# Kernel tuning notes

Measured on AMD Instinct MI355X. Metric: run time of the kernel, lower is better.

## Reference

```python
import jax, jax.numpy as jnp
import numpy as np

B, S, D, N = 8, 4096, 1024, 16
EPS = 1e-6


def setup_inputs() -> dict:
    key = jax.random.key(0)
    ks = jax.random.split(key, 6)
    s = 1.0 / np.sqrt(D)
    return {
        "x": jax.random.normal(ks[0], (B, S, D), dtype=jnp.float32),
        "W_lambda": jax.random.uniform(ks[1], (N, D), jnp.float32, -s, s),
        "b_lambda": jnp.full((N,), 2.0, dtype=jnp.float32),  # nn.init.constant_(bias, 2.0)
        "W_B": jax.random.uniform(ks[2], (N, D), jnp.float32, -s, s),
        "W_C": jax.random.uniform(ks[3], (D, N), jnp.float32, -1.0 / np.sqrt(N), 1.0 / np.sqrt(N)),
        "W_gate": jax.random.uniform(ks[4], (D, D), jnp.float32, -s, s),
        "rms_weight": jnp.ones((D,), dtype=jnp.float32),
    }


def reference(x, W_lambda, b_lambda, W_B, W_C, W_gate, rms_weight):
    # Input-dependent decay and input projection, computed for all timesteps at once
    lam = jax.nn.sigmoid(jnp.einsum("bsd,nd->bsn", x, W_lambda) + b_lambda)  # (B,S,N)
    Bx = jnp.einsum("bsd,nd->bsn", x, W_B)  # (B,S,N)

    def step(h, inp):
        l_t, b_t = inp
        h = l_t * h + b_t  # h_t = lambda_t * h_{t-1} + B_t x_t
        return h, h

    h0 = jnp.zeros((x.shape[0], W_B.shape[0]), dtype=x.dtype)
    _, hs = jax.lax.scan(step, h0, (jnp.swapaxes(lam, 0, 1), jnp.swapaxes(Bx, 0, 1)))
    hs = jnp.swapaxes(hs, 0, 1)  # (B,S,N)

    y = jnp.einsum("bsn,dn->bsd", hs, W_C)  # C @ h_t
    gate = jax.nn.sigmoid(jnp.einsum("bsd,ed->bse", x, W_gate))
    y = gate * y
    # RMSNorm
    rms = jax.lax.rsqrt(jnp.mean(y * y, axis=-1, keepdims=True) + EPS)
    return y * rms * rms_weight
```

## Files before the change

### kernel.cpp

```cpp
#include <hip/hip_runtime.h>

#define DD 1024
#define NN 16
#define SS 4096
#define BBATCH 8
#define TOK (BBATCH*SS)

typedef __attribute__((ext_vector_type(8))) __bf16 bf16x8;
typedef __attribute__((ext_vector_type(4))) float f32x4;
typedef unsigned int u32;
typedef unsigned long long u64;

__device__ __forceinline__ void async16(void* lds, const void* g) {
  __builtin_amdgcn_global_load_lds(
      (const __attribute__((address_space(1))) u32*)(u64)(g),
      (__attribute__((address_space(3))) u32*)(u32)(u64)(lds), 16, 0, 0);
}

__device__ __forceinline__ float sigmoidf_(float v) {
  return 1.f / (1.f + __expf(-v));
}

__global__ void k_cvt(const float* __restrict__ in, __bf16* __restrict__ out, int n8) {
  int i = blockIdx.x * blockDim.x + threadIdx.x;
  if (i >= n8) return;
  const float4* in4 = (const float4*)in;
  float4 a = in4[(u64)i * 2 + 0];
  float4 b = in4[(u64)i * 2 + 1];
  bf16x8 o;
  o[0] = (__bf16)a.x; o[1] = (__bf16)a.y; o[2] = (__bf16)a.z; o[3] = (__bf16)a.w;
  o[4] = (__bf16)b.x; o[5] = (__bf16)b.y; o[6] = (__bf16)b.z; o[7] = (__bf16)b.w;
  *(bf16x8*)(out + (u64)i * 8) = o;
}

__global__ __launch_bounds__(256)
void k_proj(const __bf16* __restrict__ xb, const __bf16* __restrict__ wp,
            const float* __restrict__ b_lambda,
            float* __restrict__ lam, float* __restrict__ bx) {
  __shared__ __align__(16) __bf16 sA[128 * 32];
  __shared__ __align__(16) __bf16 sB[32 * 32];
  int tid = threadIdx.x;
  int lane = tid & 63, w = tid >> 6;
  int tok0 = blockIdx.x * 128;
  u64 aSrc[2];
#pragma unroll
  for (int q = 0; q < 2; ++q) {
    int u = q * 256 + tid;
    int row = u >> 2, slot = (u & 3) ^ (row & 3);
    aSrc[q] = (u64)((const char*)xb + ((u64)(tok0 + row) * DD + slot * 8) * 2);
  }
  u64 bSrc;
  {
    int u = tid;
    int row = u >> 2, slot = (u & 3) ^ (row & 3);
    bSrc = (u64)((const char*)wp + ((u64)row * DD + slot * 8) * 2);
  }
  f32x4 acc[2][2] = {};
  int r15 = lane & 15, kg = lane >> 4;
  for (int kt = 0; kt < DD / 32; ++kt) {
#pragma unroll
    for (int q = 0; q < 2; ++q)
      async16((char*)sA + (q * 256 + w * 64) * 16, (const void*)(aSrc[q] + kt * 64));
    if (tid < 128)
      async16((char*)sB + w * 1024, (const void*)(bSrc + kt * 64));
    __syncthreads();
    bf16x8 bfr[2];
#pragma unroll
    for (int nt = 0; nt < 2; ++nt) {
      int brow = nt * 16 + r15;
      bfr[nt] = *(const bf16x8*)((const char*)sB + brow * 64 + ((kg ^ (brow & 3)) << 4));
    }
#pragma unroll
    for (int mt = 0; mt < 2; ++mt) {
      int arow = w * 32 + mt * 16 + r15;
      bf16x8 af = *(const bf16x8*)((const char*)sA + arow * 64 + ((kg ^ (arow & 3)) << 4));
#pragma unroll
      for (int nt = 0; nt < 2; ++nt)
        acc[mt][nt] = __builtin_amdgcn_mfma_f32_16x16x32_bf16(af, bfr[nt], acc[mt][nt], 0, 0, 0);
    }
    __syncthreads();
  }
#pragma unroll
  for (int mt = 0; mt < 2; ++mt)
#pragma unroll
    for (int nt = 0; nt < 2; ++nt)
#pragma unroll
      for (int r = 0; r < 4; ++r) {
        int token = tok0 + w * 32 + mt * 16 + kg * 4 + r;
        int j = nt * 16 + r15;
        float v = acc[mt][nt][r];
        if (j < 16) lam[token * NN + j] = sigmoidf_(v + b_lambda[j]);
        else        bx[token * NN + (j - 16)] = v;
      }
}

__global__ __launch_bounds__(256)
void k_scan(const float* __restrict__ lam, const float* __restrict__ bx,
            float* __restrict__ hs) {
  int b = blockIdx.x >> 4, n = blockIdx.x & 15;
  int t = threadIdx.x;
  const int CH = SS / 256;
  float lv[CH], bv[CH];
  int base = (b * SS + t * CH) * NN + n;
  float a = 1.f, bacc = 0.f;
#pragma unroll
  for (int i = 0; i < CH; ++i) {
    lv[i] = lam[base + i * NN];
    bv[i] = bx[base + i * NN];
    bacc = lv[i] * bacc + bv[i];
    a *= lv[i];
  }
  __shared__ float As[2][256], Bs[2][256];
  As[0][t] = a; Bs[0][t] = bacc;
  __syncthreads();
  int cur = 0;
  for (int off = 1; off < 256; off <<= 1) {
    float a2 = As[cur][t], b2 = Bs[cur][t];
    if (t >= off) {
      float ap = As[cur][t - off], bp = Bs[cur][t - off];
      b2 = b2 + a2 * bp;
      a2 = a2 * ap;
    }
    As[cur ^ 1][t] = a2; Bs[cur ^ 1][t] = b2;
    cur ^= 1;
    __syncthreads();
  }
  float h = (t == 0) ? 0.f : Bs[cur][t - 1];
#pragma unroll
  for (int i = 0; i < CH; ++i) {
    h = lv[i] * h + bv[i];
    hs[base + i * NN] = h;
  }
}

#define STG(kt, bi) do { u32 lb = (u32)(bi) * 32768u; u64 ko = (u64)(kt) * 64u;          \
    async16(smc + lb + (u32)w * 1024u,              (const void*)(aAddr0 + ko));         \
    async16(smc + lb + (u32)(8 + w) * 1024u,        (const void*)(aAddr1 + ko));         \
    async16(smc + lb + 16384u + (u32)w * 1024u,     (const void*)(bAddr0 + ko));         \
    async16(smc + lb + 16384u + (u32)(8 + w) * 1024u,(const void*)(bAddr1 + ko)); } while (0)

__global__ __launch_bounds__(512, 2)
void k_gemm(const __bf16* __restrict__ xb, const __bf16* __restrict__ wg,
            const float* __restrict__ hs, const float* __restrict__ wc,
            float* __restrict__ out) {
  __shared__ __align__(16) char smc[131072];
  const int tid = threadIdx.x, lane = tid & 63, w = tid >> 6;
  const int r15 = lane & 15, kg = lane >> 4;
  const int wr = w >> 2, wcq = w & 3;
  int bid = blockIdx.x;
  int swz = (bid & 7) * 64 + (bid >> 3);
  int m = swz >> 2, n = swz & 3;
  const int tok0 = m * 256, n0 = n * 256;
  const int sslot = (lane & 3) ^ ((lane >> 2) & 3) ^ ((lane >> 4) & 3);
  const int rA0 = w * 16 + (lane >> 2);
  const int rA1 = (8 + w) * 16 + (lane >> 2);
  const u64 aAddr0 = (u64)(const char*)xb + (u64)(tok0 + rA0) * 2048 + (u32)sslot * 16;
  const u64 aAddr1 = (u64)(const char*)xb + (u64)(tok0 + rA1) * 2048 + (u32)sslot * 16;
  const u64 bAddr0 = (u64)(const char*)wg + (u64)(n0 + rA0) * 2048 + (u32)sslot * 16;
  const u64 bAddr1 = (u64)(const char*)wg + (u64)(n0 + rA1) * 2048 + (u32)sslot * 16;

  f32x4 acc[8][4] = {};

  STG(0, 0); STG(1, 1); STG(2, 2);
  asm volatile("s_waitcnt vmcnt(8)" ::: "memory");
  __builtin_amdgcn_s_barrier();
  __builtin_amdgcn_sched_barrier(0);

  for (int t = 0; t < 32; ++t) {
    if (t + 3 < 32) STG(t + 3, (t + 3) & 3);
    const char* Ab = smc + (t & 3) * 32768;
    const char* Bb = Ab + 16384;
    bf16x8 af[8];
#pragma unroll
    for (int mt = 0; mt < 8; ++mt) {
      int row = wr * 128 + mt * 16 + r15;
      int sl = kg ^ (row & 3) ^ ((row >> 2) & 3);
      af[mt] = *(const bf16x8*)(Ab + row * 64 + sl * 16);
    }
    __builtin_amdgcn_s_setprio(1);
#pragma unroll
    for (int nt = 0; nt < 4; ++nt) {
      int brow = wcq * 64 + nt * 16 + r15;
      int sl = kg ^ (brow & 3) ^ ((brow >> 2) & 3);
      bf16x8 bfr = *(const bf16x8*)(Bb + brow * 64 + sl * 16);
#pragma unroll
      for (int mt = 0; mt < 8; ++mt)
        acc[mt][nt] = __builtin_amdgcn_mfma_f32_16x16x32_bf16(af[mt], bfr, acc[mt][nt], 0, 0, 0);
    }
    __builtin_amdgcn_s_setprio(0);
    if (t < 29)       asm volatile("s_waitcnt vmcnt(8)" ::: "memory");
    else if (t == 29) asm volatile("s_waitcnt vmcnt(4)" ::: "memory");
    else              asm volatile("s_waitcnt vmcnt(0)" ::: "memory");
    __builtin_amdgcn_s_barrier();
    __builtin_amdgcn_sched_barrier(0);
  }

  float* hsl = (float*)smc;
  float* wcl = (float*)(smc + 16384);
  for (int idx = tid; idx < 256 * 16; idx += 512) hsl[idx] = hs[(u64)tok0 * NN + idx];
  for (int idx = tid; idx < 256 * 16; idx += 512) wcl[idx] = wc[(u64)n0 * NN + idx];
  __syncthreads();
  f32x4 wcv[4][4];
#pragma unroll
  for (int nt = 0; nt < 4; ++nt) {
    int j = wcq * 64 + nt * 16 + r15;
#pragma unroll
    for (int q = 0; q < 4; ++q) wcv[nt][q] = *(const f32x4*)(wcl + j * 16 + q * 4);
  }
#pragma unroll
  for (int mt = 0; mt < 8; ++mt)
#pragma unroll
    for (int r = 0; r < 4; ++r) {
      int i = wr * 128 + mt * 16 + kg * 4 + r;
      f32x4 hv[4];
#pragma unroll
      for (int q = 0; q < 4; ++q) hv[q] = *(const f32x4*)(hsl + i * 16 + q * 4);
#pragma unroll
      for (int nt = 0; nt < 4; ++nt) {
        f32x4 cv = hv[0] * wcv[nt][0];
        cv += hv[1] * wcv[nt][1];
        cv += hv[2] * wcv[nt][2];
        cv += hv[3] * wcv[nt][3];
        float cy = cv[0] + cv[1] + cv[2] + cv[3];
        float g = sigmoidf_(acc[mt][nt][r]);
        int j = wcq * 64 + nt * 16 + r15;
        out[(u64)(tok0 + i) * DD + n0 + j] = g * cy;
      }
    }
}

__global__ __launch_bounds__(256)
void k_norm(float* __restrict__ out, const float* __restrict__ rw) {
  int row = blockIdx.x * 4 + (threadIdx.x >> 6);
  int lane = threadIdx.x & 63;
  float4* p = (float4*)(out + (u64)row * DD);
  float4 v[4];
  float rs = 0.f;
#pragma unroll
  for (int e = 0; e < 4; ++e) {
    v[e] = p[e * 64 + lane];
    rs += v[e].x * v[e].x + v[e].y * v[e].y + v[e].z * v[e].z + v[e].w * v[e].w;
  }
#pragma unroll
  for (int msk = 1; msk < 64; msk <<= 1) rs += __shfl_xor(rs, msk, 64);
  float rstd = rsqrtf(rs * (1.f / DD) + 1e-6f);
  const float4* rwp = (const float4*)rw;
#pragma unroll
  for (int e = 0; e < 4; ++e) {
    float4 wv = rwp[e * 64 + lane];
    float4 o;
    o.x = v[e].x * rstd * wv.x;
    o.y = v[e].y * rstd * wv.y;
    o.z = v[e].z * rstd * wv.z;
    o.w = v[e].w * rstd * wv.w;
    p[e * 64 + lane] = o;
  }
}

extern "C" void kernel_launch(void* const* d_in, const int* in_sizes, int n_in,
                              void* d_out, int out_size, void* d_ws, size_t ws_size,
                              hipStream_t stream) {
  (void)in_sizes; (void)n_in; (void)out_size; (void)ws_size;
  const float* x        = (const float*)d_in[0];
  const float* W_lambda = (const float*)d_in[1];
  const float* b_lambda = (const float*)d_in[2];
  const float* W_B      = (const float*)d_in[3];
  const float* W_C      = (const float*)d_in[4];
  const float* W_gate   = (const float*)d_in[5];
  const float* rms_w    = (const float*)d_in[6];
  char* ws = (char*)d_ws;
  __bf16* xb  = (__bf16*)(ws + 0);
  __bf16* wg  = (__bf16*)(ws + 67108864);
  __bf16* wp  = (__bf16*)(ws + 69206016);
  float*  lam = (float*)(ws + 69271552);
  float*  bx  = (float*)(ws + 71368704);
  float*  hs  = (float*)(ws + 73465856);
  float*  out = (float*)d_out;

  k_cvt<<<TOK * DD / 8 / 256, 256, 0, stream>>>(x, xb, TOK * DD / 8);
  k_cvt<<<DD * DD / 8 / 256, 256, 0, stream>>>(W_gate, wg, DD * DD / 8);
  k_cvt<<<NN * DD / 8 / 256, 256, 0, stream>>>(W_lambda, wp, NN * DD / 8);
  k_cvt<<<NN * DD / 8 / 256, 256, 0, stream>>>(W_B, wp + NN * DD, NN * DD / 8);
  k_proj<<<TOK / 128, 256, 0, stream>>>(xb, wp, b_lambda, lam, bx);
  k_scan<<<BBATCH * NN, 256, 0, stream>>>(lam, bx, hs);
  k_gemm<<<(TOK / 256) * (DD / 256), 512, 0, stream>>>(xb, wg, hs, W_C, out);
  k_norm<<<TOK / 4, 256, 0, stream>>>(out, rms_w);
}
```

Baseline: 209.7 us.

## Fuse x conversion into projection and store gated output as bf16 intermediate

The separate fp32-to-bf16 conversion of x is folded into the projection kernel, which reads fp32 x, writes the bf16 copy for the big GEMM and fills shared memory directly. The three weight conversions are merged into one launch. When the workspace is large enough, the GEMM epilogue writes the gated output as bf16 to a scratch buffer and a new norm kernel reads it, which halves intermediate traffic but adds a bf16 rounding before the RMSNorm. The hs and W_C shared-memory tiles are padded to a stride of 20 to reduce bank conflicts.

Measured after the change: 206.2 us. About the same (-1.7%).

```diff
diff --git a/kernel.cpp b/kernel.cpp
--- a/kernel.cpp
+++ b/kernel.cpp
@@ -7,6 +7,7 @@
 #define TOK (BBATCH*SS)
 
 typedef __attribute__((ext_vector_type(8))) __bf16 bf16x8;
+typedef __attribute__((ext_vector_type(4))) __bf16 bf16x4;
 typedef __attribute__((ext_vector_type(4))) float f32x4;
 typedef unsigned int u32;
 typedef unsigned long long u64;
@@ -21,34 +22,36 @@
   return 1.f / (1.f + __expf(-v));
 }
 
-__global__ void k_cvt(const float* __restrict__ in, __bf16* __restrict__ out, int n8) {
+__global__ void k_cvtw(const float* __restrict__ wgf, const float* __restrict__ wlf,
+                       const float* __restrict__ wbf, __bf16* __restrict__ wg,
+                       __bf16* __restrict__ wp) {
   int i = blockIdx.x * blockDim.x + threadIdx.x;
-  if (i >= n8) return;
-  const float4* in4 = (const float4*)in;
-  float4 a = in4[(u64)i * 2 + 0];
-  float4 b = in4[(u64)i * 2 + 1];
+  const int NG = DD * DD / 8, NP = NN * DD / 8;
+  const float* src; __bf16* dst;
+  if (i < NG)           { src = wgf + (u64)i * 8;            dst = wg + (u64)i * 8; }
+  else if (i < NG + NP) { int j = i - NG; src = wlf + j * 8; dst = wp + j * 8; }
+  else if (i < NG + 2 * NP) { int j = i - NG - NP; src = wbf + j * 8; dst = wp + NN * DD + j * 8; }
+  else return;
+  float4 a = *(const float4*)src, b = *(const float4*)(src + 4);
   bf16x8 o;
   o[0] = (__bf16)a.x; o[1] = (__bf16)a.y; o[2] = (__bf16)a.z; o[3] = (__bf16)a.w;
   o[4] = (__bf16)b.x; o[5] = (__bf16)b.y; o[6] = (__bf16)b.z; o[7] = (__bf16)b.w;
-  *(bf16x8*)(out + (u64)i * 8) = o;
+  *(bf16x8*)dst = o;
 }
 
 __global__ __launch_bounds__(256)
-void k_proj(const __bf16* __restrict__ xb, const __bf16* __restrict__ wp,
-            const float* __restrict__ b_lambda,
+void k_proj(const float* __restrict__ x, const __bf16* __restrict__ wp,
+            const float* __restrict__ b_lambda, __bf16* __restrict__ xb,
             float* __restrict__ lam, float* __restrict__ bx) {
   __shared__ __align__(16) __bf16 sA[128 * 32];
   __shared__ __align__(16) __bf16 sB[32 * 32];
   int tid = threadIdx.x;
   int lane = tid & 63, w = tid >> 6;
   int tok0 = blockIdx.x * 128;
-  u64 aSrc[2];
-#pragma unroll
-  for (int q = 0; q < 2; ++q) {
-    int u = q * 256 + tid;
-    int row = u >> 2, slot = (u & 3) ^ (row & 3);
-    aSrc[q] = (u64)((const char*)xb + ((u64)(tok0 + row) * DD + slot * 8) * 2);
-  }
+  int crow = tid >> 1, cs = (tid & 1) * 2;
+  const float* xsrc = x + (u64)(tok0 + crow) * DD + (tid & 1) * 16;
+  __bf16* xdst = xb + (u64)(tok0 + crow) * DD + (tid & 1) * 16;
+  int sw = (crow & 3) ^ ((crow >> 2) & 3);
   u64 bSrc;
   {
     int u = tid;
@@ -58,9 +61,19 @@
   f32x4 acc[2][2] = {};
   int r15 = lane & 15, kg = lane >> 4;
   for (int kt = 0; kt < DD / 32; ++kt) {
-#pragma unroll
-    for (int q = 0; q < 2; ++q)
-      async16((char*)sA + (q * 256 + w * 64) * 16, (const void*)(aSrc[q] + kt * 64));
+    float4 a0 = *(const float4*)(xsrc + kt * 32 + 0);
+    float4 a1 = *(const float4*)(xsrc + kt * 32 + 4);
+    float4 a2 = *(const float4*)(xsrc + kt * 32 + 8);
+    float4 a3 = *(const float4*)(xsrc + kt * 32 + 12);
+    bf16x8 lo, hi;
+    lo[0] = (__bf16)a0.x; lo[1] = (__bf16)a0.y; lo[2] = (__bf16)a0.z; lo[3] = (__bf16)a0.w;
+    lo[4] = (__bf16)a1.x; lo[5] = (__bf16)a1.y; lo[6] = (__bf16)a1.z; lo[7] = (__bf16)a1.w;
+    hi[0] = (__bf16)a2.x; hi[1] = (__bf16)a2.y; hi[2] = (__bf16)a2.z; hi[3] = (__bf16)a2.w;
+    hi[4] = (__bf16)a3.x; hi[5] = (__bf16)a3.y; hi[6] = (__bf16)a3.z; hi[7] = (__bf16)a3.w;
+    *(bf16x8*)(xdst + kt * 32) = lo;
+    *(bf16x8*)(xdst + kt * 32 + 8) = hi;
+    *(bf16x8*)((char*)sA + crow * 64 + ((cs ^ sw) << 4)) = lo;
+    *(bf16x8*)((char*)sA + crow * 64 + (((cs + 1) ^ sw) << 4)) = hi;
     if (tid < 128)
       async16((char*)sB + w * 1024, (const void*)(bSrc + kt * 64));
     __syncthreads();
@@ -73,7 +86,8 @@
 #pragma unroll
     for (int mt = 0; mt < 2; ++mt) {
       int arow = w * 32 + mt * 16 + r15;
-      bf16x8 af = *(const bf16x8*)((const char*)sA + arow * 64 + ((kg ^ (arow & 3)) << 4));
+      bf16x8 af = *(const bf16x8*)((const char*)sA + arow * 64 +
+                                   ((kg ^ (arow & 3) ^ ((arow >> 2) & 3)) << 4));
 #pragma unroll
       for (int nt = 0; nt < 2; ++nt)
         acc[mt][nt] = __builtin_amdgcn_mfma_f32_16x16x32_bf16(af, bfr[nt], acc[mt][nt], 0, 0, 0);
@@ -139,10 +153,11 @@
     async16(smc + lb + 16384u + (u32)w * 1024u,     (const void*)(bAddr0 + ko));         \
     async16(smc + lb + 16384u + (u32)(8 + w) * 1024u,(const void*)(bAddr1 + ko)); } while (0)
 
+template<int YB16>
 __global__ __launch_bounds__(512, 2)
 void k_gemm(const __bf16* __restrict__ xb, const __bf16* __restrict__ wg,
             const float* __restrict__ hs, const float* __restrict__ wc,
-            float* __restrict__ out) {
+            float* __restrict__ outf, __bf16* __restrict__ outb) {
   __shared__ __align__(16) char smc[131072];
   const int tid = threadIdx.x, lane = tid & 63, w = tid >> 6;
   const int r15 = lane & 15, kg = lane >> 4;
@@ -196,16 +211,19 @@
   }
 
   float* hsl = (float*)smc;
-  float* wcl = (float*)(smc + 16384);
-  for (int idx = tid; idx < 256 * 16; idx += 512) hsl[idx] = hs[(u64)tok0 * NN + idx];
-  for (int idx = tid; idx < 256 * 16; idx += 512) wcl[idx] = wc[(u64)n0 * NN + idx];
+  float* wcl = (float*)(smc + 20480);
+  for (int idx = tid; idx < 256 * 16; idx += 512) {
+    int r = idx >> 4, c = idx & 15;
+    hsl[r * 20 + c] = hs[(u64)tok0 * NN + idx];
+    wcl[r * 20 + c] = wc[(u64)n0 * NN + idx];
+  }
   __syncthreads();
   f32x4 wcv[4][4];
 #pragma unroll
   for (int nt = 0; nt < 4; ++nt) {
     int j = wcq * 64 + nt * 16 + r15;
 #pragma unroll
-    for (int q = 0; q < 4; ++q) wcv[nt][q] = *(const f32x4*)(wcl + j * 16 + q * 4);
+    for (int q = 0; q < 4; ++q) wcv[nt][q] = *(const f32x4*)(wcl + j * 20 + q * 4);
   }
 #pragma unroll
   for (int mt = 0; mt < 8; ++mt)
@@ -214,7 +232,7 @@
       int i = wr * 128 + mt * 16 + kg * 4 + r;
       f32x4 hv[4];
 #pragma unroll
-      for (int q = 0; q < 4; ++q) hv[q] = *(const f32x4*)(hsl + i * 16 + q * 4);
+      for (int q = 0; q < 4; ++q) hv[q] = *(const f32x4*)(hsl + i * 20 + q * 4);
 #pragma unroll
       for (int nt = 0; nt < 4; ++nt) {
         f32x4 cv = hv[0] * wcv[nt][0];
@@ -224,13 +242,49 @@
         float cy = cv[0] + cv[1] + cv[2] + cv[3];
         float g = sigmoidf_(acc[mt][nt][r]);
         int j = wcq * 64 + nt * 16 + r15;
-        out[(u64)(tok0 + i) * DD + n0 + j] = g * cy;
+        u64 off = (u64)(tok0 + i) * DD + n0 + j;
+        if (YB16) outb[off] = (__bf16)(g * cy);
+        else      outf[off] = g * cy;
       }
     }
 }
 
 __global__ __launch_bounds__(256)
-void k_norm(float* __restrict__ out, const float* __restrict__ rw) {
+void k_norm_b(const __bf16* __restrict__ yb, float* __restrict__ out,
+              const float* __restrict__ rw) {
+  int row = blockIdx.x * 4 + (threadIdx.x >> 6);
+  int lane = threadIdx.x & 63;
+  const __bf16* yrow = yb + (u64)row * DD;
+  bf16x4 v[4];
+  float f[16];
+  float rs = 0.f;
+#pragma unroll
+  for (int q = 0; q < 4; ++q) {
+    v[q] = *(const bf16x4*)(yrow + q * 256 + lane * 4);
+#pragma unroll
+    for (int e = 0; e < 4; ++e) {
+      f[q * 4 + e] = (float)v[q][e];
+      rs += f[q * 4 + e] * f[q * 4 + e];
+    }
+  }
+#pragma unroll
+  for (int msk = 1; msk < 64; msk <<= 1) rs += __shfl_xor(rs, msk, 64);
+  float rstd = rsqrtf(rs * (1.f / DD) + 1e-6f);
+  float* orow = out + (u64)row * DD;
+#pragma unroll
+  for (int q = 0; q < 4; ++q) {
+    float4 wv = *(const float4*)(rw + q * 256 + lane * 4);
+    float4 o;
+    o.x = f[q * 4 + 0] * rstd * wv.x;
+    o.y = f[q * 4 + 1] * rstd * wv.y;
+    o.z = f[q * 4 + 2] * rstd * wv.z;
+    o.w = f[q * 4 + 3] * rstd * wv.w;
+    *(float4*)(orow + q * 256 + lane * 4) = o;
+  }
+}
+
+__global__ __launch_bounds__(256)
+void k_norm_f(float* __restrict__ out, const float* __restrict__ rw) {
   int row = blockIdx.x * 4 + (threadIdx.x >> 6);
   int lane = threadIdx.x & 63;
   float4* p = (float4*)(out + (u64)row * DD);
@@ -260,7 +314,7 @@
 extern "C" void kernel_launch(void* const* d_in, const int* in_sizes, int n_in,
                               void* d_out, int out_size, void* d_ws, size_t ws_size,
                               hipStream_t stream) {
-  (void)in_sizes; (void)n_in; (void)out_size; (void)ws_size;
+  (void)in_sizes; (void)n_in; (void)out_size;
   const float* x        = (const float*)d_in[0];
   const float* W_lambda = (const float*)d_in[1];
   const float* b_lambda = (const float*)d_in[2];
@@ -275,14 +329,19 @@
   float*  lam = (float*)(ws + 69271552);
   float*  bx  = (float*)(ws + 71368704);
   float*  hs  = (float*)(ws + 73465856);
+  __bf16* yb  = (__bf16*)(ws + 75563008);
   float*  out = (float*)d_out;
-
-  k_cvt<<<TOK * DD / 8 / 256, 256, 0, stream>>>(x, xb, TOK * DD / 8);
-  k_cvt<<<DD * DD / 8 / 256, 256, 0, stream>>>(W_gate, wg, DD * DD / 8);
-  k_cvt<<<NN * DD / 8 / 256, 256, 0, stream>>>(W_lambda, wp, NN * DD / 8);
-  k_cvt<<<NN * DD / 8 / 256, 256, 0, stream>>>(W_B, wp + NN * DD, NN * DD / 8);
-  k_proj<<<TOK / 128, 256, 0, stream>>>(xb, wp, b_lambda, lam, bx);
+  bool yb16 = ws_size >= (size_t)(75563008ull + 67108864ull);
+
+  k_cvtw<<<(DD * DD / 8 + 2 * NN * DD / 8 + 255) / 256, 256, 0, stream>>>(
+      W_gate, W_lambda, W_B, wg, wp);
+  k_proj<<<TOK / 128, 256, 0, stream>>>(x, wp, b_lambda, xb, lam, bx);
   k_scan<<<BBATCH * NN, 256, 0, stream>>>(lam, bx, hs);
-  k_gemm<<<(TOK / 256) * (DD / 256), 512, 0, stream>>>(xb, wg, hs, W_C, out);
-  k_norm<<<TOK / 4, 256, 0, stream>>>(out, rms_w);
-}
+  if (yb16) {
+    k_gemm<1><<<(TOK / 256) * (DD / 256), 512, 0, stream>>>(xb, wg, hs, W_C, nullptr, yb);
+    k_norm_b<<<TOK / 4, 256, 0, stream>>>(yb, out, rms_w);
+  } else {
+    k_gemm<0><<<(TOK / 256) * (DD / 256), 512, 0, stream>>>(xb, wg, hs, W_C, out, nullptr);
+    k_norm_f<<<TOK / 4, 256, 0, stream>>>(out, rms_w);
+  }
+}
```
